# Performance work log

Measured on AMD Instinct MI355X. Metric: run time of the kernel, lower is better.

The kernel has to match this reference:

```python
import jax, jax.numpy as jnp
import numpy as np

N_EMBD = 2048
N_HEAD = 8          # config.n_head // 2
HEAD_DIM = 256      # n_embd // (n_head // 2)
HALF = HEAD_DIM // 2
LAMBDA_INIT = 0.8
RMS_EPS = 1.1920929e-07  # torch float32 finfo eps (F.rms_norm default)


def _rms_norm(x):
    # F.rms_norm with no weight: x / sqrt(mean(x^2) + eps)
    return x * jax.lax.rsqrt(jnp.mean(x * x, axis=-1, keepdims=True) + RMS_EPS)


def setup_inputs() -> dict:
    key = jax.random.key(0)
    ks = jax.random.split(key, 10)
    B, T, C = 2, 2048, N_EMBD
    x = jax.random.normal(ks[0], (B, T, C), dtype=jnp.float32)
    wq = jax.random.normal(ks[1], (C, C), dtype=jnp.float32) * 0.02
    wk = jax.random.normal(ks[2], (C, C), dtype=jnp.float32) * 0.02
    wv = jax.random.normal(ks[3], (C, C), dtype=jnp.float32) * 0.02
    wo = jax.random.normal(ks[4], (C, C), dtype=jnp.float32) * 0.02
    lq1 = jax.random.normal(ks[5], (HEAD_DIM,), dtype=jnp.float32) * 0.1
    lk1 = jax.random.normal(ks[6], (HEAD_DIM,), dtype=jnp.float32) * 0.1
    lq2 = jax.random.normal(ks[7], (HEAD_DIM,), dtype=jnp.float32) * 0.1
    lk2 = jax.random.normal(ks[8], (HEAD_DIM,), dtype=jnp.float32) * 0.1
    return {"x": x, "wq": wq, "wk": wk, "wv": wv, "wo": wo,
            "lq1": lq1, "lk1": lk1, "lq2": lq2, "lk2": lk2}


def _causal_attn(q, k, v, mask):
    # q,k: [B,H,T,half], v: [B,H,T,HEAD_DIM]
    scale = 1.0 / jnp.sqrt(jnp.asarray(q.shape[-1], q.dtype))
    scores = jnp.einsum('bhqd,bhkd->bhqk', q, k) * scale
    scores = jnp.where(mask, scores, -jnp.inf)
    attn = jax.nn.softmax(scores, axis=-1)
    return jnp.einsum('bhqk,bhkd->bhqd', attn, v)


def reference(x, wq, wk, wv, wo, lq1, lk1, lq2, lk2):
    B, T, C = x.shape
    lambda_1 = jnp.exp(jnp.sum(lq1 * lk1))
    lambda_2 = jnp.exp(jnp.sum(lq2 * lk2))
    lambda_full = lambda_1 - lambda_2 + LAMBDA_INIT

    q = (x @ wq.T).reshape(B, T, N_HEAD, 2, HALF).transpose(0, 2, 1, 3, 4)  # [B,H,T,2,half]
    k = (x @ wk.T).reshape(B, T, N_HEAD, 2, HALF).transpose(0, 2, 1, 3, 4)
    v = (x @ wv.T).reshape(B, T, N_HEAD, HEAD_DIM).transpose(0, 2, 1, 3)    # [B,H,T,hd]

    q1 = _rms_norm(q[..., 0, :]); q2 = _rms_norm(q[..., 1, :])
    k1 = _rms_norm(k[..., 0, :]); k2 = _rms_norm(k[..., 1, :])

    mask = jnp.tril(jnp.ones((T, T), dtype=bool))
    y1 = _causal_attn(q1, k1, v, mask)
    y2 = _causal_attn(q2, k2, v, mask)
    y = y1 - lambda_full * y2                                               # [B,H,T,hd]

    y = y.transpose(0, 2, 1, 3).reshape(B, T, C)
    return (y @ wo.T) * (1.0 - LAMBDA_INIT)
```

## Files before the change

kernel.cpp:

```cpp
#include <hip/hip_runtime.h>
#include <stdint.h>


typedef __bf16 bf16;
typedef bf16 bf16x8 __attribute__((ext_vector_type(8)));
typedef bf16 bf16x4 __attribute__((ext_vector_type(4)));
typedef float f32x4 __attribute__((ext_vector_type(4)));

typedef void __attribute__((address_space(1)))* gas_t;
typedef void __attribute__((address_space(3)))* las_t;

__device__ __forceinline__ void gload16(const void* g, void* l) {
  __builtin_amdgcn_global_load_lds((gas_t)(uintptr_t)g, (las_t)(uint32_t)(uintptr_t)l, 16, 0, 0);
}

__device__ __forceinline__ f32x4 mfma16x16(bf16x8 a, bf16x8 b, f32x4 c) {
  return __builtin_amdgcn_mfma_f32_16x16x32_bf16(a, b, c, 0, 0, 0);
}

__global__ __launch_bounds__(256) void cast_all(const float* __restrict__ x,
                                                const float* __restrict__ wq, const float* __restrict__ wk,
                                                const float* __restrict__ wv, const float* __restrict__ wo,
                                                const float* __restrict__ lq1, const float* __restrict__ lk1,
                                                const float* __restrict__ lq2, const float* __restrict__ lk2,
                                                bf16* __restrict__ xb,
                                                bf16* __restrict__ wqb, bf16* __restrict__ wkb,
                                                bf16* __restrict__ wvb, bf16* __restrict__ wob,
                                                float* __restrict__ lam) {
  __shared__ float red[8];
  int tid = threadIdx.x;
  int i = blockIdx.x * 256 + tid;
  const float* in;
  bf16* out;
  int j;
  if (i < 2097152) {
    in = x; out = xb; j = i;
  } else {
    int k = i - 2097152;
    int w = k >> 20;
    j = k & 1048575;
    in = (w == 0) ? wq : (w == 1) ? wk : (w == 2) ? wv : wo;
    out = (w == 0) ? wqb : (w == 1) ? wkb : (w == 2) ? wvb : wob;
  }
  float4 v = ((const float4*)in)[j];
  bf16x4 o;
  o[0] = (bf16)v.x; o[1] = (bf16)v.y; o[2] = (bf16)v.z; o[3] = (bf16)v.w;
  ((bf16x4*)out)[j] = o;

  if (blockIdx.x == 0) {
    float a = lq1[tid] * lk1[tid];
    float b = lq2[tid] * lk2[tid];
#pragma unroll
    for (int m = 32; m >= 1; m >>= 1) {
      a += __shfl_xor(a, m, 64);
      b += __shfl_xor(b, m, 64);
    }
    if ((tid & 63) == 0) { red[tid >> 6] = a; red[4 + (tid >> 6)] = b; }
    __syncthreads();
    if (tid == 0) {
      float s1 = red[0] + red[1] + red[2] + red[3];
      float s2 = red[4] + red[5] + red[6] + red[7];
      lam[0] = expf(s1) - expf(s2) + 0.8f;
    }
  }
}

__global__ __launch_bounds__(512, 2) void gemm_qkv8(const bf16* __restrict__ A,
                                                    const bf16* __restrict__ Bq,
                                                    const bf16* __restrict__ Bk,
                                                    const bf16* __restrict__ Bv,
                                                    bf16* __restrict__ Cq, bf16* __restrict__ Ck,
                                                    bf16* __restrict__ Cv) {
  __shared__ char lds[98304];
  const int K = 2048, nt = 64;

  int p = blockIdx.y * gridDim.x + blockIdx.x;
  int lid = (p & 7) * 48 + (p >> 3);
  const int bm = (lid / 24) * 256;
  const int bnG = (lid % 24) * 256;
  const int z = bnG >> 11;
  const int bn = bnG & 2047;
  const bf16* B = (z == 0) ? Bq : ((z == 1) ? Bk : Bv);

  const int tid = threadIdx.x;
  const int wid = tid >> 6, lane = tid & 63;
  const int l15 = lane & 15, lhi = lane >> 4;
  const int wm = wid >> 2, wn = wid & 3;

  const bf16* aS0 = A + (size_t)(bm + wid * 16 + l15) * K + lhi * 8;
  const bf16* bS0 = B + (size_t)(bn + wid * 16 + l15) * K + lhi * 8;

  auto stA = [&](int t, int pb) {
    char* d = lds + pb * 32768 + wid * 1024;
    const bf16* s = aS0 + t * 32;
    gload16(s, d);
    gload16(s + (size_t)128 * K, d + 8192);
  };
  auto stB = [&](int t, int pb) {
    char* d = lds + pb * 32768 + 16384 + wid * 1024;
    const bf16* s = bS0 + t * 32;
    gload16(s, d);
    gload16(s + (size_t)128 * K, d + 8192);
  };

  const f32x4 fz = {0.f, 0.f, 0.f, 0.f};
  f32x4 acc[8][4];
#pragma unroll
  for (int m = 0; m < 8; ++m)
#pragma unroll
    for (int n = 0; n < 4; ++n) acc[m][n] = fz;

  stA(0, 0); stB(0, 0);
  stA(1, 1); stB(1, 1);
  asm volatile("s_waitcnt vmcnt(4)" ::: "memory");
  __builtin_amdgcn_s_barrier();

  int cur = 0;
  for (int t = 0; t < nt; ++t) {
    const char* ab = lds + cur * 32768;
    const char* bb = ab + 16384;
    int nx2 = cur + 2; if (nx2 >= 3) nx2 -= 3;
    bf16x8 a[8], b0, b1;

#pragma unroll
    for (int m = 0; m < 8; ++m) a[m] = *(const bf16x8*)(ab + (wm * 8 + m) * 1024 + lane * 16);
    b0 = *(const bf16x8*)(bb + (wn * 4 + 0) * 1024 + lane * 16);
    b1 = *(const bf16x8*)(bb + (wn * 4 + 1) * 1024 + lane * 16);
    if (t + 2 < nt) stA(t + 2, nx2);
    __builtin_amdgcn_s_barrier();
    __builtin_amdgcn_s_setprio(1);
#pragma unroll
    for (int m = 0; m < 8; ++m) {
      acc[m][0] = mfma16x16(a[m], b0, acc[m][0]);
      acc[m][1] = mfma16x16(a[m], b1, acc[m][1]);
    }
    __builtin_amdgcn_s_setprio(0);
    __builtin_amdgcn_s_barrier();

    b0 = *(const bf16x8*)(bb + (wn * 4 + 2) * 1024 + lane * 16);
    b1 = *(const bf16x8*)(bb + (wn * 4 + 3) * 1024 + lane * 16);
    if (t + 2 < nt) stB(t + 2, nx2);
    __builtin_amdgcn_s_barrier();
    __builtin_amdgcn_s_setprio(1);
#pragma unroll
    for (int m = 0; m < 8; ++m) {
      acc[m][2] = mfma16x16(a[m], b0, acc[m][2]);
      acc[m][3] = mfma16x16(a[m], b1, acc[m][3]);
    }
    __builtin_amdgcn_s_setprio(0);
    if (t + 2 < nt) {
      asm volatile("s_waitcnt vmcnt(4)" ::: "memory");
    } else {
      asm volatile("s_waitcnt vmcnt(0)" ::: "memory");
    }
    __builtin_amdgcn_s_barrier();

    cur = (cur == 2) ? 0 : cur + 1;
  }

  if (z == 2) {
#pragma unroll
    for (int m = 0; m < 8; ++m)
#pragma unroll
      for (int n = 0; n < 4; ++n)
#pragma unroll
        for (int r = 0; r < 4; ++r) {
          int row = bm + wm * 128 + m * 16 + lhi * 4 + r;
          int col = bn + wn * 64 + n * 16 + l15;
          int bb3 = row >> 11, tt = row & 2047;
          Cv[(size_t)bb3 * 2048 * 2048 + (size_t)col * 2048 + tt] = (bf16)acc[m][n][r];
        }
    return;
  }
  float* ldsf = (float*)lds;
#pragma unroll
  for (int m = 0; m < 8; ++m)
#pragma unroll
    for (int r = 0; r < 4; ++r) {
      float s = acc[m][0][r] * acc[m][0][r] + acc[m][1][r] * acc[m][1][r] +
                acc[m][2][r] * acc[m][2][r] + acc[m][3][r] * acc[m][3][r];
      s += __shfl_xor(s, 1, 64);
      s += __shfl_xor(s, 2, 64);
      s += __shfl_xor(s, 4, 64);
      s += __shfl_xor(s, 8, 64);
      if (l15 == 0) ldsf[(wm * 128 + m * 16 + lhi * 4 + r) * 4 + wn] = s;
    }
  __syncthreads();
  const float osc = (z == 0) ? 0.08838834764831845f : 1.0f;
  bf16* C = (z == 0) ? Cq : Ck;
#pragma unroll
  for (int m = 0; m < 8; ++m) {
#pragma unroll
    for (int r = 0; r < 4; ++r) {
      int rl = wm * 128 + m * 16 + lhi * 4 + r;
      float tot = ldsf[rl * 4 + (wn & 2)] + ldsf[rl * 4 + (wn & 2) + 1];
      float sc = rsqrtf(tot * (1.0f / 128.0f) + 1.1920929e-07f) * osc;
#pragma unroll
      for (int n = 0; n < 4; ++n) {
        int col = bn + wn * 64 + n * 16 + l15;
        C[(size_t)(bm + rl) * 2048 + col] = (bf16)(acc[m][n][r] * sc);
      }
    }
  }
}

__global__ __launch_bounds__(512) void gemm_out(const bf16* __restrict__ A, const bf16* __restrict__ B,
                                                float* __restrict__ Cf) {
  __shared__ char lds[73728];
  const int K = 2048, nt = 64;

  int p = blockIdx.x;
  int lid = (p & 7) * 32 + (p >> 3);
  const int bm = (lid >> 4) * 256;
  const int bn = (lid & 15) * 128;

  const int tid = threadIdx.x;
  const int wid = tid >> 6, lane = tid & 63;
  const int l15 = lane & 15, lhi = lane >> 4;
  const int wm = wid >> 1, wn = wid & 1;

  const bf16* aB = A + (size_t)(bm + wid * 16 + l15) * K + lhi * 8;
  const bf16* bB = B + (size_t)(bn + wid * 16 + l15) * K + lhi * 8;

  auto stage = [&](int t, int pb) {
    char* base = lds + pb * 24576;
    const int k0 = t * 32;
    gload16(aB + k0, base + wid * 1024);
    gload16(aB + (size_t)128 * K + k0, base + 8192 + wid * 1024);
    gload16(bB + k0, base + 16384 + wid * 1024);
  };

  const f32x4 fz = {0.f, 0.f, 0.f, 0.f};
  f32x4 acc[4][4];
#pragma unroll
  for (int m = 0; m < 4; ++m)
#pragma unroll
    for (int n = 0; n < 4; ++n) acc[m][n] = fz;

  stage(0, 0);
  stage(1, 1);
  asm volatile("s_waitcnt vmcnt(3)" ::: "memory");
  __builtin_amdgcn_s_barrier();

  for (int t = 0; t < nt; ++t) {
    const char* ab = lds + (t % 3) * 24576;
    if (t + 2 < nt) stage(t + 2, (t + 2) % 3);
    bf16x8 a[4], b[4];
#pragma unroll
    for (int m = 0; m < 4; ++m)
      a[m] = *(const bf16x8*)(ab + (wm * 4 + m) * 1024 + lane * 16);
#pragma unroll
    for (int n = 0; n < 4; ++n)
      b[n] = *(const bf16x8*)(ab + 16384 + (wn * 4 + n) * 1024 + lane * 16);
    __builtin_amdgcn_s_setprio(1);
#pragma unroll
    for (int m = 0; m < 4; ++m)
#pragma unroll
      for (int n = 0; n < 4; ++n) acc[m][n] = mfma16x16(a[m], b[n], acc[m][n]);
    __builtin_amdgcn_s_setprio(0);
    if (t + 2 < nt) {
      asm volatile("s_waitcnt vmcnt(3)" ::: "memory");
    } else {
      asm volatile("s_waitcnt vmcnt(0)" ::: "memory");
    }
    __builtin_amdgcn_s_barrier();
  }

#pragma unroll
  for (int m = 0; m < 4; ++m)
#pragma unroll
    for (int n = 0; n < 4; ++n)
#pragma unroll
      for (int r = 0; r < 4; ++r) {
        int row = bm + wm * 64 + m * 16 + lhi * 4 + r;
        int col = bn + wn * 64 + n * 16 + l15;
        Cf[(size_t)row * 2048 + col] = acc[m][n][r] * 0.2f;
      }
}

__global__ __launch_bounds__(256) void attn_kernel(const bf16* __restrict__ qb, const bf16* __restrict__ kb,
                                                   const bf16* __restrict__ vtb, bf16* __restrict__ yb,
                                                   const float* __restrict__ lamp) {
  __shared__ char lds[73728];
  const int tid = threadIdx.x;
  const int wid = tid >> 6, lane = tid & 63;
  const int l15 = lane & 15, lhi = lane >> 4;
  char* pl = lds + 65536 + wid * 2048;
  const int s = wid >> 1;
  const int rg = wid & 1;

  const int p = blockIdx.x;
  const int bh = p & 15;
  const int qt = (p < 256) ? (31 - (p >> 4)) : ((p - 256) >> 4);
  const int b = bh >> 3, h = bh & 7;
  const int wr0 = qt * 64 + rg * 32;
  const float lam = lamp[0];

  bf16x8 qf[2][4];
#pragma unroll
  for (int rf = 0; rf < 2; ++rf) {
    const bf16* qrow = qb + (size_t)(b * 2048 + wr0 + rf * 16 + l15) * 2048 + h * 256 + s * 128 + lhi * 8;
#pragma unroll
    for (int c = 0; c < 4; ++c) qf[rf][c] = *(const bf16x8*)(qrow + c * 32);
  }

  const f32x4 fz = {0.f, 0.f, 0.f, 0.f};
  f32x4 y[2][16];
#pragma unroll
  for (int rf = 0; rf < 2; ++rf)
#pragma unroll
    for (int f = 0; f < 16; ++f) y[rf][f] = fz;
  float lsum[2][4] = {{0.f, 0.f, 0.f, 0.f}, {0.f, 0.f, 0.f, 0.f}};

  const int nkt = 2 * qt + 2;
  const bf16* kbase = kb + (size_t)(b * 2048) * 2048 + h * 256;
  const bf16* vbase = vtb + (size_t)b * 2048 * 2048 + (size_t)(h * 256) * 2048;

  auto stageK = [&](int kt2, int pp) {
    const int t0 = kt2 * 32;
    char* kd = lds + pp * 16384 + wid * 1024;
    const bf16* sp = kbase + (size_t)(t0 + l15) * 2048 + wid * 32 + lhi * 8;
    gload16(sp, kd);
    gload16(sp + 16 * 2048, kd + 4096);
    gload16(sp + 128, kd + 8192);
    gload16(sp + 16 * 2048 + 128, kd + 12288);
  };
  auto stageVT = [&](int kt2, int pp) {
    const int t0 = kt2 * 32;
    char* vd = lds + 32768 + pp * 16384;
    const bf16* vp = vbase + (size_t)(wid * 16 + l15) * 2048 + t0 + lhi * 8;
#pragma unroll
    for (int i = 0; i < 4; ++i)
      gload16(vp + (size_t)i * 64 * 2048, vd + (i * 4 + wid) * 1024);
  };

  stageK(0, 0);
  stageVT(0, 0);
  __syncthreads();

  for (int kt = 0; kt < nkt; ++kt) {
    const int cur = kt & 1;
    const int t0 = kt * 32;
    const bool active = (t0 <= wr0 + 31);
    if (kt + 1 < nkt) {
      stageK(kt + 1, cur ^ 1);
      stageVT(kt + 1, cur ^ 1);
    }
    if (active) {
      const char* kc = lds + cur * 16384 + s * 8192;
      const char* vc = lds + 32768 + cur * 16384;
      f32x4 sg[2][2];
      __builtin_amdgcn_s_setprio(1);
#pragma unroll
      for (int rf = 0; rf < 2; ++rf)
#pragma unroll
        for (int g = 0; g < 2; ++g) {
          f32x4 a = fz;
#pragma unroll
          for (int ks = 0; ks < 4; ++ks)
            a = mfma16x16(qf[rf][ks], *(const bf16x8*)(kc + ((g * 4 + ks) * 64 + lane) * 16), a);
          sg[rf][g] = a;
        }
      __builtin_amdgcn_s_setprio(0);
      if (t0 + 31 > wr0) {
#pragma unroll
        for (int rf = 0; rf < 2; ++rf)
#pragma unroll
          for (int g = 0; g < 2; ++g) {
            int col = t0 + g * 16 + l15;
#pragma unroll
            for (int r = 0; r < 4; ++r) {
              int row = wr0 + rf * 16 + lhi * 4 + r;
              if (col > row) sg[rf][g][r] = -1e30f;
            }
          }
      }
#pragma unroll
      for (int rf = 0; rf < 2; ++rf)
#pragma unroll
        for (int g = 0; g < 2; ++g)
#pragma unroll
          for (int r = 0; r < 4; ++r) {
            float pv = __expf(sg[rf][g][r] - 12.0f);
            lsum[rf][r] += pv;
            *(bf16*)(pl + rf * 1024 + ((lhi * 4 + r) * 32 + g * 16 + l15) * 2) = (bf16)pv;
          }
      bf16x8 pa0 = *(const bf16x8*)(pl + (l15 * 32 + lhi * 8) * 2);
      bf16x8 pa1 = *(const bf16x8*)(pl + 1024 + (l15 * 32 + lhi * 8) * 2);
      __builtin_amdgcn_s_setprio(1);
#pragma unroll
      for (int f = 0; f < 16; ++f) {
        bf16x8 vf = *(const bf16x8*)(vc + (f * 64 + lane) * 16);
        y[0][f] = mfma16x16(pa0, vf, y[0][f]);
        y[1][f] = mfma16x16(pa1, vf, y[1][f]);
      }
      __builtin_amdgcn_s_setprio(0);
    }
    __syncthreads();
  }

  float inv[2][4];
#pragma unroll
  for (int rf = 0; rf < 2; ++rf)
#pragma unroll
    for (int r = 0; r < 4; ++r) {
      float sv = lsum[rf][r];
      sv += __shfl_xor(sv, 1, 64);
      sv += __shfl_xor(sv, 2, 64);
      sv += __shfl_xor(sv, 4, 64);
      sv += __shfl_xor(sv, 8, 64);
      inv[rf][r] = (s == 0) ? (1.f / sv) : (lam / sv);
    }
  float* yx = (float*)lds;
  if (s == 0) {
#pragma unroll
    for (int rf = 0; rf < 2; ++rf)
#pragma unroll
      for (int f = 0; f < 16; ++f)
#pragma unroll
        for (int r = 0; r < 4; ++r) {
          int rl = rg * 32 + rf * 16 + lhi * 4 + r;
          yx[rl * 256 + f * 16 + l15] = y[rf][f][r] * inv[rf][r];
        }
  }
  __syncthreads();
  if (s == 1) {
#pragma unroll
    for (int rf = 0; rf < 2; ++rf)
#pragma unroll
      for (int r = 0; r < 4; ++r) {
        int rl = rg * 32 + rf * 16 + lhi * 4 + r;
        bf16* orow = yb + (size_t)(b * 2048 + qt * 64 + rl) * 2048 + h * 256 + l15;
#pragma unroll
        for (int f = 0; f < 16; ++f) {
          float v = yx[rl * 256 + f * 16 + l15] - y[rf][f][r] * inv[rf][r];
          orow[f * 16] = (bf16)v;
        }
      }
  }
}

extern "C" void kernel_launch(void* const* d_in, const int* in_sizes, int n_in,
                              void* d_out, int out_size, void* d_ws, size_t ws_size,
                              hipStream_t stream) {
  const float* x = (const float*)d_in[0];
  const float* wq = (const float*)d_in[1];
  const float* wk = (const float*)d_in[2];
  const float* wv = (const float*)d_in[3];
  const float* wo = (const float*)d_in[4];
  const float* lq1 = (const float*)d_in[5];
  const float* lk1 = (const float*)d_in[6];
  const float* lq2 = (const float*)d_in[7];
  const float* lk2 = (const float*)d_in[8];
  float* out = (float*)d_out;
  char* ws = (char*)d_ws;

  if (ws_size < 117440516) return;

  bf16* xb = (bf16*)(ws + 0);
  bf16* wqb = (bf16*)(ws + 16777216);
  bf16* wkb = (bf16*)(ws + 25165824);
  bf16* wvb = (bf16*)(ws + 33554432);
  bf16* wob = (bf16*)(ws + 41943040);
  bf16* qbuf = (bf16*)(ws + 50331648);
  bf16* kbuf = (bf16*)(ws + 67108864);
  bf16* vtb = (bf16*)(ws + 83886080);
  bf16* ybuf = (bf16*)(ws + 100663296);
  float* lam = (float*)(ws + 117440512);

  cast_all<<<24576, 256, 0, stream>>>(x, wq, wk, wv, wo, lq1, lk1, lq2, lk2,
                                      xb, wqb, wkb, wvb, wob, lam);

  gemm_qkv8<<<dim3(24, 16), 512, 0, stream>>>(xb, wqb, wkb, wvb, qbuf, kbuf, vtb);

  attn_kernel<<<512, 256, 0, stream>>>(qbuf, kbuf, vtb, ybuf, lam);

  gemm_out<<<256, 512, 0, stream>>>(ybuf, wob, out);
}
```

Baseline: 339.8 us.

## Load K/V fragments directly from global memory and remap blocks per XCD

Measured after the change: 400.4 us. 17.8% more time.

```diff
diff --git a/kernel.cpp b/kernel.cpp
--- a/kernel.cpp
+++ b/kernel.cpp
@@ -281,17 +281,18 @@
 __global__ __launch_bounds__(256) void attn_kernel(const bf16* __restrict__ qb, const bf16* __restrict__ kb,
                                                    const bf16* __restrict__ vtb, bf16* __restrict__ yb,
                                                    const float* __restrict__ lamp) {
-  __shared__ char lds[73728];
+  __shared__ char lds[65536];
   const int tid = threadIdx.x;
   const int wid = tid >> 6, lane = tid & 63;
   const int l15 = lane & 15, lhi = lane >> 4;
-  char* pl = lds + 65536 + wid * 2048;
+  char* pl = lds + wid * 2048;
   const int s = wid >> 1;
   const int rg = wid & 1;
 
   const int p = blockIdx.x;
-  const int bh = p & 15;
-  const int qt = (p < 256) ? (31 - (p >> 4)) : ((p - 256) >> 4);
+  const int xcd = p & 7, r = p >> 3;
+  const int bh = xcd * 2 + (r & 1);
+  const int qt = 31 - (r >> 1);
   const int b = bh >> 3, h = bh & 7;
   const int wr0 = qt * 64 + rg * 32;
   const float lam = lamp[0];
@@ -313,43 +314,20 @@
   float lsum[2][4] = {{0.f, 0.f, 0.f, 0.f}, {0.f, 0.f, 0.f, 0.f}};
 
   const int nkt = 2 * qt + 2;
-  const bf16* kbase = kb + (size_t)(b * 2048) * 2048 + h * 256;
-  const bf16* vbase = vtb + (size_t)b * 2048 * 2048 + (size_t)(h * 256) * 2048;
-
-  auto stageK = [&](int kt2, int pp) {
-    const int t0 = kt2 * 32;
-    char* kd = lds + pp * 16384 + wid * 1024;
-    const bf16* sp = kbase + (size_t)(t0 + l15) * 2048 + wid * 32 + lhi * 8;
-    gload16(sp, kd);
-    gload16(sp + 16 * 2048, kd + 4096);
-    gload16(sp + 128, kd + 8192);
-    gload16(sp + 16 * 2048 + 128, kd + 12288);
-  };
-  auto stageVT = [&](int kt2, int pp) {
-    const int t0 = kt2 * 32;
-    char* vd = lds + 32768 + pp * 16384;
-    const bf16* vp = vbase + (size_t)(wid * 16 + l15) * 2048 + t0 + lhi * 8;
-#pragma unroll
-    for (int i = 0; i < 4; ++i)
-      gload16(vp + (size_t)i * 64 * 2048, vd + (i * 4 + wid) * 1024);
-  };
-
-  stageK(0, 0);
-  stageVT(0, 0);
-  __syncthreads();
+  const bf16* kfb = kb + (size_t)(b * 2048 + l15) * 2048 + h * 256 + s * 128 + lhi * 8;
+  const bf16* vfb = vtb + (size_t)b * 2048 * 2048 + (size_t)(h * 256 + l15) * 2048 + lhi * 8;
 
   for (int kt = 0; kt < nkt; ++kt) {
-    const int cur = kt & 1;
     const int t0 = kt * 32;
     const bool active = (t0 <= wr0 + 31);
-    if (kt + 1 < nkt) {
-      stageK(kt + 1, cur ^ 1);
-      stageVT(kt + 1, cur ^ 1);
-    }
     if (active) {
-      const char* kc = lds + cur * 16384 + s * 8192;
-      const char* vc = lds + 32768 + cur * 16384;
       f32x4 sg[2][2];
+      bf16x8 kf[2][4];
+#pragma unroll
+      for (int g = 0; g < 2; ++g)
+#pragma unroll
+        for (int ks = 0; ks < 4; ++ks)
+          kf[g][ks] = *(const bf16x8*)(kfb + (size_t)(t0 + g * 16) * 2048 + ks * 32);
       __builtin_amdgcn_s_setprio(1);
 #pragma unroll
       for (int rf = 0; rf < 2; ++rf)
@@ -357,8 +335,7 @@
         for (int g = 0; g < 2; ++g) {
           f32x4 a = fz;
 #pragma unroll
-          for (int ks = 0; ks < 4; ++ks)
-            a = mfma16x16(qf[rf][ks], *(const bf16x8*)(kc + ((g * 4 + ks) * 64 + lane) * 16), a);
+          for (int ks = 0; ks < 4; ++ks) a = mfma16x16(qf[rf][ks], kf[g][ks], a);
           sg[rf][g] = a;
         }
       __builtin_amdgcn_s_setprio(0);
@@ -369,9 +346,9 @@
           for (int g = 0; g < 2; ++g) {
             int col = t0 + g * 16 + l15;
 #pragma unroll
-            for (int r = 0; r < 4; ++r) {
-              int row = wr0 + rf * 16 + lhi * 4 + r;
-              if (col > row) sg[rf][g][r] = -1e30f;
+            for (int r2 = 0; r2 < 4; ++r2) {
+              int row = wr0 + rf * 16 + lhi * 4 + r2;
+              if (col > row) sg[rf][g][r2] = -1e30f;
             }
           }
       }
@@ -380,37 +357,37 @@
 #pragma unroll
         for (int g = 0; g < 2; ++g)
 #pragma unroll
-          for (int r = 0; r < 4; ++r) {
-            float pv = __expf(sg[rf][g][r] - 12.0f);
-            lsum[rf][r] += pv;
-            *(bf16*)(pl + rf * 1024 + ((lhi * 4 + r) * 32 + g * 16 + l15) * 2) = (bf16)pv;
+          for (int r2 = 0; r2 < 4; ++r2) {
+            float pv = __expf(sg[rf][g][r2]);
+            lsum[rf][r2] += pv;
+            *(bf16*)(pl + rf * 1024 + ((lhi * 4 + r2) * 32 + g * 16 + l15) * 2) = (bf16)pv;
           }
       bf16x8 pa0 = *(const bf16x8*)(pl + (l15 * 32 + lhi * 8) * 2);
       bf16x8 pa1 = *(const bf16x8*)(pl + 1024 + (l15 * 32 + lhi * 8) * 2);
       __builtin_amdgcn_s_setprio(1);
 #pragma unroll
       for (int f = 0; f < 16; ++f) {
-        bf16x8 vf = *(const bf16x8*)(vc + (f * 64 + lane) * 16);
+        bf16x8 vf = *(const bf16x8*)(vfb + (size_t)(f * 16) * 2048 + t0);
         y[0][f] = mfma16x16(pa0, vf, y[0][f]);
         y[1][f] = mfma16x16(pa1, vf, y[1][f]);
       }
       __builtin_amdgcn_s_setprio(0);
     }
-    __syncthreads();
   }
 
   float inv[2][4];
 #pragma unroll
   for (int rf = 0; rf < 2; ++rf)
 #pragma unroll
-    for (int r = 0; r < 4; ++r) {
-      float sv = lsum[rf][r];
+    for (int r2 = 0; r2 < 4; ++r2) {
+      float sv = lsum[rf][r2];
       sv += __shfl_xor(sv, 1, 64);
       sv += __shfl_xor(sv, 2, 64);
       sv += __shfl_xor(sv, 4, 64);
       sv += __shfl_xor(sv, 8, 64);
-      inv[rf][r] = (s == 0) ? (1.f / sv) : (lam / sv);
-    }
+      inv[rf][r2] = (s == 0) ? (1.f / sv) : (lam / sv);
+    }
+  __syncthreads();
   float* yx = (float*)lds;
   if (s == 0) {
 #pragma unroll
@@ -418,9 +395,9 @@
 #pragma unroll
       for (int f = 0; f < 16; ++f)
 #pragma unroll
-        for (int r = 0; r < 4; ++r) {
-          int rl = rg * 32 + rf * 16 + lhi * 4 + r;
-          yx[rl * 256 + f * 16 + l15] = y[rf][f][r] * inv[rf][r];
+        for (int r2 = 0; r2 < 4; ++r2) {
+          int rl = rg * 32 + rf * 16 + lhi * 4 + r2;
+          yx[rl * 256 + f * 16 + l15] = y[rf][f][r2] * inv[rf][r2];
         }
   }
   __syncthreads();
@@ -428,12 +405,12 @@
 #pragma unroll
     for (int rf = 0; rf < 2; ++rf)
 #pragma unroll
-      for (int r = 0; r < 4; ++r) {
-        int rl = rg * 32 + rf * 16 + lhi * 4 + r;
+      for (int r2 = 0; r2 < 4; ++r2) {
+        int rl = rg * 32 + rf * 16 + lhi * 4 + r2;
         bf16* orow = yb + (size_t)(b * 2048 + qt * 64 + rl) * 2048 + h * 256 + l15;
 #pragma unroll
         for (int f = 0; f < 16; ++f) {
-          float v = yx[rl * 256 + f * 16 + l15] - y[rf][f][r] * inv[rf][r];
+          float v = yx[rl * 256 + f * 16 + l15] - y[rf][f][r2] * inv[rf][r2];
           orow[f * 16] = (bf16)v;
         }
       }
```

## Split attention work across 8 waves with 16 query rows each

Applied to the files above, without the earlier changes.

Result: faster. 301.5 us, median of 2 (-11.3%).

```diff
diff --git a/kernel.cpp b/kernel.cpp
--- a/kernel.cpp
+++ b/kernel.cpp
@@ -278,165 +278,145 @@
       }
 }
 
-__global__ __launch_bounds__(256) void attn_kernel(const bf16* __restrict__ qb, const bf16* __restrict__ kb,
-                                                   const bf16* __restrict__ vtb, bf16* __restrict__ yb,
-                                                   const float* __restrict__ lamp) {
+__global__ __launch_bounds__(512, 4) void attn_kernel(const bf16* __restrict__ qb, const bf16* __restrict__ kb,
+                                                      const bf16* __restrict__ vtb, bf16* __restrict__ yb,
+                                                      const float* __restrict__ lamp) {
   __shared__ char lds[73728];
   const int tid = threadIdx.x;
   const int wid = tid >> 6, lane = tid & 63;
   const int l15 = lane & 15, lhi = lane >> 4;
-  char* pl = lds + 65536 + wid * 2048;
-  const int s = wid >> 1;
-  const int rg = wid & 1;
+  char* pl = lds + 65536 + wid * 1024;
+  const int s = wid >> 2;
+  const int rg = wid & 3;
 
   const int p = blockIdx.x;
   const int bh = p & 15;
   const int qt = (p < 256) ? (31 - (p >> 4)) : ((p - 256) >> 4);
   const int b = bh >> 3, h = bh & 7;
-  const int wr0 = qt * 64 + rg * 32;
+  const int wr0 = qt * 64 + rg * 16;
   const float lam = lamp[0];
 
-  bf16x8 qf[2][4];
-#pragma unroll
-  for (int rf = 0; rf < 2; ++rf) {
-    const bf16* qrow = qb + (size_t)(b * 2048 + wr0 + rf * 16 + l15) * 2048 + h * 256 + s * 128 + lhi * 8;
-#pragma unroll
-    for (int c = 0; c < 4; ++c) qf[rf][c] = *(const bf16x8*)(qrow + c * 32);
+  bf16x8 qf[4];
+  {
+    const bf16* qrow = qb + (size_t)(b * 2048 + wr0 + l15) * 2048 + h * 256 + s * 128 + lhi * 8;
+#pragma unroll
+    for (int c = 0; c < 4; ++c) qf[c] = *(const bf16x8*)(qrow + c * 32);
   }
 
   const f32x4 fz = {0.f, 0.f, 0.f, 0.f};
-  f32x4 y[2][16];
-#pragma unroll
-  for (int rf = 0; rf < 2; ++rf)
-#pragma unroll
-    for (int f = 0; f < 16; ++f) y[rf][f] = fz;
-  float lsum[2][4] = {{0.f, 0.f, 0.f, 0.f}, {0.f, 0.f, 0.f, 0.f}};
+  f32x4 y[16];
+#pragma unroll
+  for (int f = 0; f < 16; ++f) y[f] = fz;
+  float lsum[4] = {0.f, 0.f, 0.f, 0.f};
 
   const int nkt = 2 * qt + 2;
   const bf16* kbase = kb + (size_t)(b * 2048) * 2048 + h * 256;
   const bf16* vbase = vtb + (size_t)b * 2048 * 2048 + (size_t)(h * 256) * 2048;
 
-  auto stageK = [&](int kt2, int pp) {
+  auto stage = [&](int kt2, int pp) {
     const int t0 = kt2 * 32;
-    char* kd = lds + pp * 16384 + wid * 1024;
-    const bf16* sp = kbase + (size_t)(t0 + l15) * 2048 + wid * 32 + lhi * 8;
-    gload16(sp, kd);
-    gload16(sp + 16 * 2048, kd + 4096);
-    gload16(sp + 128, kd + 8192);
-    gload16(sp + 16 * 2048 + 128, kd + 12288);
+#pragma unroll
+    for (int c = 0; c < 2; ++c) {
+      int cc = wid * 2 + c;
+      int ss = cc >> 3, tg = (cc >> 2) & 1, kc = cc & 3;
+      const bf16* sp = kbase + (size_t)(t0 + tg * 16 + l15) * 2048 + ss * 128 + kc * 32 + lhi * 8;
+      gload16(sp, lds + pp * 16384 + ss * 8192 + tg * 4096 + kc * 1024);
+    }
+#pragma unroll
+    for (int c = 0; c < 2; ++c) {
+      int cc = wid * 2 + c;
+      int i = cc >> 2, w4 = cc & 3;
+      const bf16* vp = vbase + (size_t)(i * 64 + w4 * 16 + l15) * 2048 + t0 + lhi * 8;
+      gload16(vp, lds + 32768 + pp * 16384 + cc * 1024);
+    }
   };
-  auto stageVT = [&](int kt2, int pp) {
-    const int t0 = kt2 * 32;
-    char* vd = lds + 32768 + pp * 16384;
-    const bf16* vp = vbase + (size_t)(wid * 16 + l15) * 2048 + t0 + lhi * 8;
-#pragma unroll
-    for (int i = 0; i < 4; ++i)
-      gload16(vp + (size_t)i * 64 * 2048, vd + (i * 4 + wid) * 1024);
-  };
-
-  stageK(0, 0);
-  stageVT(0, 0);
+
+  stage(0, 0);
   __syncthreads();
 
   for (int kt = 0; kt < nkt; ++kt) {
     const int cur = kt & 1;
     const int t0 = kt * 32;
-    const bool active = (t0 <= wr0 + 31);
-    if (kt + 1 < nkt) {
-      stageK(kt + 1, cur ^ 1);
-      stageVT(kt + 1, cur ^ 1);
-    }
+    const bool active = (t0 <= wr0 + 15);
+    if (kt + 1 < nkt) stage(kt + 1, cur ^ 1);
     if (active) {
       const char* kc = lds + cur * 16384 + s * 8192;
       const char* vc = lds + 32768 + cur * 16384;
-      f32x4 sg[2][2];
+      f32x4 sg[2];
       __builtin_amdgcn_s_setprio(1);
 #pragma unroll
-      for (int rf = 0; rf < 2; ++rf)
-#pragma unroll
-        for (int g = 0; g < 2; ++g) {
-          f32x4 a = fz;
-#pragma unroll
-          for (int ks = 0; ks < 4; ++ks)
-            a = mfma16x16(qf[rf][ks], *(const bf16x8*)(kc + ((g * 4 + ks) * 64 + lane) * 16), a);
-          sg[rf][g] = a;
-        }
+      for (int g = 0; g < 2; ++g) {
+        f32x4 a = fz;
+#pragma unroll
+        for (int ks = 0; ks < 4; ++ks)
+          a = mfma16x16(qf[ks], *(const bf16x8*)(kc + (g * 4096 + ks * 1024) + lane * 16), a);
+        sg[g] = a;
+      }
       __builtin_amdgcn_s_setprio(0);
       if (t0 + 31 > wr0) {
 #pragma unroll
-        for (int rf = 0; rf < 2; ++rf)
-#pragma unroll
-          for (int g = 0; g < 2; ++g) {
-            int col = t0 + g * 16 + l15;
-#pragma unroll
-            for (int r = 0; r < 4; ++r) {
-              int row = wr0 + rf * 16 + lhi * 4 + r;
-              if (col > row) sg[rf][g][r] = -1e30f;
-            }
+        for (int g = 0; g < 2; ++g) {
+          int col = t0 + g * 16 + l15;
+#pragma unroll
+          for (int r = 0; r < 4; ++r) {
+            int row = wr0 + lhi * 4 + r;
+            if (col > row) sg[g][r] = -1e30f;
           }
-      }
-#pragma unroll
-      for (int rf = 0; rf < 2; ++rf)
-#pragma unroll
-        for (int g = 0; g < 2; ++g)
-#pragma unroll
-          for (int r = 0; r < 4; ++r) {
-            float pv = __expf(sg[rf][g][r] - 12.0f);
-            lsum[rf][r] += pv;
-            *(bf16*)(pl + rf * 1024 + ((lhi * 4 + r) * 32 + g * 16 + l15) * 2) = (bf16)pv;
-          }
-      bf16x8 pa0 = *(const bf16x8*)(pl + (l15 * 32 + lhi * 8) * 2);
-      bf16x8 pa1 = *(const bf16x8*)(pl + 1024 + (l15 * 32 + lhi * 8) * 2);
+        }
+      }
+#pragma unroll
+      for (int g = 0; g < 2; ++g)
+#pragma unroll
+        for (int r = 0; r < 4; ++r) {
+          float pv = __expf(sg[g][r] - 12.0f);
+          lsum[r] += pv;
+          *(bf16*)(pl + ((lhi * 4 + r) * 32 + g * 16 + l15) * 2) = (bf16)pv;
+        }
+      bf16x8 pa = *(const bf16x8*)(pl + (l15 * 32 + lhi * 8) * 2);
       __builtin_amdgcn_s_setprio(1);
 #pragma unroll
       for (int f = 0; f < 16; ++f) {
         bf16x8 vf = *(const bf16x8*)(vc + (f * 64 + lane) * 16);
-        y[0][f] = mfma16x16(pa0, vf, y[0][f]);
-        y[1][f] = mfma16x16(pa1, vf, y[1][f]);
+        y[f] = mfma16x16(pa, vf, y[f]);
       }
       __builtin_amdgcn_s_setprio(0);
     }
     __syncthreads();
   }
 
-  float inv[2][4];
-#pragma unroll
-  for (int rf = 0; rf < 2; ++rf)
-#pragma unroll
-    for (int r = 0; r < 4; ++r) {
-      float sv = lsum[rf][r];
-      sv += __shfl_xor(sv, 1, 64);
-      sv += __shfl_xor(sv, 2, 64);
-      sv += __shfl_xor(sv, 4, 64);
-      sv += __shfl_xor(sv, 8, 64);
-      inv[rf][r] = (s == 0) ? (1.f / sv) : (lam / sv);
-    }
+  float inv[4];
+#pragma unroll
+  for (int r = 0; r < 4; ++r) {
+    float sv = lsum[r];
+    sv += __shfl_xor(sv, 1, 64);
+    sv += __shfl_xor(sv, 2, 64);
+    sv += __shfl_xor(sv, 4, 64);
+    sv += __shfl_xor(sv, 8, 64);
+    inv[r] = (s == 0) ? (1.f / sv) : (lam / sv);
+  }
+  __syncthreads();
   float* yx = (float*)lds;
   if (s == 0) {
 #pragma unroll
-    for (int rf = 0; rf < 2; ++rf)
-#pragma unroll
-      for (int f = 0; f < 16; ++f)
-#pragma unroll
-        for (int r = 0; r < 4; ++r) {
-          int rl = rg * 32 + rf * 16 + lhi * 4 + r;
-          yx[rl * 256 + f * 16 + l15] = y[rf][f][r] * inv[rf][r];
-        }
+    for (int f = 0; f < 16; ++f)
+#pragma unroll
+      for (int r = 0; r < 4; ++r) {
+        int rl = rg * 16 + lhi * 4 + r;
+        yx[rl * 256 + f * 16 + l15] = y[f][r] * inv[r];
+      }
   }
   __syncthreads();
   if (s == 1) {
 #pragma unroll
-    for (int rf = 0; rf < 2; ++rf)
-#pragma unroll
-      for (int r = 0; r < 4; ++r) {
-        int rl = rg * 32 + rf * 16 + lhi * 4 + r;
-        bf16* orow = yb + (size_t)(b * 2048 + qt * 64 + rl) * 2048 + h * 256 + l15;
-#pragma unroll
-        for (int f = 0; f < 16; ++f) {
-          float v = yx[rl * 256 + f * 16 + l15] - y[rf][f][r] * inv[rf][r];
-          orow[f * 16] = (bf16)v;
-        }
-      }
+    for (int r = 0; r < 4; ++r) {
+      int rl = rg * 16 + lhi * 4 + r;
+      bf16* orow = yb + (size_t)(b * 2048 + qt * 64 + rl) * 2048 + h * 256 + l15;
+#pragma unroll
+      for (int f = 0; f < 16; ++f) {
+        float v = yx[rl * 256 + f * 16 + l15] - y[f][r] * inv[r];
+        orow[f * 16] = (bf16)v;
+      }
+    }
   }
 }
 
@@ -473,7 +453,7 @@
 
   gemm_qkv8<<<dim3(24, 16), 512, 0, stream>>>(xb, wqb, wkb, wvb, qbuf, kbuf, vtb);
 
-  attn_kernel<<<512, 256, 0, stream>>>(qbuf, kbuf, vtb, ybuf, lam);
+  attn_kernel<<<512, 512, 0, stream>>>(qbuf, kbuf, vtb, ybuf, lam);
 
   gemm_out<<<256, 512, 0, stream>>>(ybuf, wob, out);
 }
```
